# Performance work log

Measured on AMD Instinct MI355X. Metric: run time of the kernel, lower is better.

Reference implementation:

```python
import jax, jax.numpy as jnp
import numpy as np

B_BATCH, N_ATOMS, N_CGS = 128, 512, 16


def setup_inputs() -> dict:
    key = jax.random.key(0)
    k0, k1, k2, k3, k4, k5 = jax.random.split(key, 6)
    npair = N_CGS * N_CGS
    soft_assign = jax.random.uniform(k0, (B_BATCH, N_ATOMS, N_CGS), dtype=jnp.float32)
    a = jax.random.uniform(k1, (B_BATCH, N_ATOMS, N_CGS), dtype=jnp.float32)
    assign_norm = a / a.sum(axis=-1, keepdims=True)  # row-normalized soft assignment
    xyz = jax.random.normal(k2, (B_BATCH, N_ATOMS, 3), dtype=jnp.float32)
    cg_xyz = jax.random.normal(k3, (B_BATCH, N_CGS, 3), dtype=jnp.float32)
    W = 0.01 * jax.random.normal(k4, (N_ATOMS, npair + npair * npair), dtype=jnp.float32)
    assign_idx = jax.random.randint(k5, (N_ATOMS,), 0, N_CGS)
    return {"soft_assign": soft_assign, "xyz": xyz, "cg_xyz": cg_xyz,
            "assign_norm": assign_norm, "W": W, "assign_idx": assign_idx}


def reference(soft_assign, xyz, cg_xyz, assign_norm, W, assign_idx):
    b, n_cgs = cg_xyz.shape[0], cg_xyz.shape[1]
    npair = n_cgs * n_cgs
    # pairwise displacement basis: basis[b,i,j] = cg_xyz[b,j] - cg_xyz[b,i]
    basis = cg_xyz[:, None, :, :] - cg_xyz[:, :, None, :]      # [b, nc, nc, 3]
    Bmat = basis.reshape(b, npair, 3)                          # [b, npair, 3]
    # cross basis: entry (p,q) = cross(Bmat[q], Bmat[p]) (matches torch Bij x Bjk)
    cross_basis = jnp.cross(Bmat[:, None, :, :], Bmat[:, :, None, :])  # [b,npair,npair,3]
    Bfull = jnp.concatenate([Bmat, cross_basis.reshape(b, npair * npair, 3)], axis=1)
    # dx_recon[b,n,e] = sum_j Bfull[b,j,e] * W[n,j]
    dx_recon = jnp.einsum('bje,nj->bne', Bfull, W)             # [b, n_atoms, 3]
    # per-CG mean offset weighted by soft assignment
    cg_offset = jnp.einsum('bin,bij->bjn', dx_recon, assign_norm)  # [b, n_cgs, 3]
    xyz_recon = cg_xyz[:, assign_idx, :] - cg_offset[:, assign_idx, :] + dx_recon
    return (soft_assign, xyz, xyz_recon)
```

## Files before the change

### kernel.cpp

```cpp
#include <hip/hip_runtime.h>

constexpr int NC = 16;
constexpr int NP = 256;
constexpr int PITCH = 264;
constexpr int NATOMS = 512;
constexpr int NB = 128;
constexpr int WROW = NP + NP * NP;

__global__ __launch_bounds__(256) void k_stream(const float* __restrict__ W,
                                                const float* __restrict__ soft_assign,
                                                const float* __restrict__ xyz,
                                                float* __restrict__ wcd_part,
                                                float* __restrict__ out_sa,
                                                float* __restrict__ out_xyz) {
    __shared__ float Hl[NC][PITCH];
    const int bid = blockIdx.x;
    const int n = bid >> 1;
    const int half = bid & 1;
    const int t = threadIdx.x;

    ((float4*)out_sa)[bid * 256 + t] = ((const float4*)soft_assign)[bid * 256 + t];
    if (t < 48) {
        ((float4*)out_xyz)[bid * 48 + t] = ((const float4*)xyz)[bid * 48 + t];
    }

    const float* __restrict__ wp =
        W + (size_t)n * WROW + NP + (size_t)(half * 128) * NP + t;
    float h[NC];
#pragma unroll
    for (int d = 0; d < NC; ++d) h[d] = 0.f;
    float hn[8];
#pragma unroll
    for (int g = 0; g < 8; ++g) {
        float s = 0.f;
#pragma unroll
        for (int i = 0; i < 16; ++i) {
            const float v = wp[(size_t)(g * 16 + i) * NP];
            h[i] += v;
            s += v;
        }
        hn[g] = s;
    }
    if (half == 0) {
        h[0] -= hn[0]; h[1] -= hn[1]; h[2] -= hn[2]; h[3] -= hn[3];
        h[4] -= hn[4]; h[5] -= hn[5]; h[6] -= hn[6]; h[7] -= hn[7];
    } else {
        h[8]  -= hn[0]; h[9]  -= hn[1]; h[10] -= hn[2]; h[11] -= hn[3];
        h[12] -= hn[4]; h[13] -= hn[5]; h[14] -= hn[6]; h[15] -= hn[7];
    }

#pragma unroll
    for (int d = 0; d < NC; ++d) Hl[d][t] = h[d];
    __syncthreads();

    {
        const int d = t >> 4, c = t & 15;
        float rp = 0.f, rm = 0.f;
#pragma unroll
        for (int qi = 0; qi < NC; ++qi) rp += Hl[d][qi * NC + c];
#pragma unroll
        for (int qj = 0; qj < NC; ++qj) rm += Hl[d][c * NC + qj];
        wcd_part[((size_t)half * NATOMS + n) * NP + t] = rp - rm;
    }
}

__global__ __launch_bounds__(256) void k_sum(const float* __restrict__ wcd_part,
                                             const float* __restrict__ W,
                                             float* __restrict__ wcd,
                                             float* __restrict__ w1c) {
    const int n = blockIdx.x;
    const int t = threadIdx.x;
    const float a = wcd_part[(size_t)n * NP + t] +
                    wcd_part[((size_t)NATOMS + n) * NP + t];
    wcd[n * NP + t] = a;
    if (t < NC) {
        const float* __restrict__ W1 = W + (size_t)n * WROW;
        float a1 = 0.f;
#pragma unroll
        for (int pi = 0; pi < NC; ++pi) a1 += W1[pi * NC + t];
#pragma unroll
        for (int pj = 0; pj < NC; ++pj) a1 -= W1[t * NC + pj];
        w1c[n * NC + t] = a1;
    }
}

__global__ __launch_bounds__(512) void k_recon(const float* __restrict__ cg_xyz,
                                               const float* __restrict__ assign_norm,
                                               const int* __restrict__ assign_idx,
                                               const float* __restrict__ wcd,
                                               const float* __restrict__ w1c,
                                               float* __restrict__ out_recon) {
    __shared__ float xs[NC][4];
    __shared__ float cxs[NP][4];
    __shared__ float part[8][48];
    __shared__ float cgo[48];
    const int b = blockIdx.x;
    const int t = threadIdx.x;

    if (t < NC * 3) xs[t / 3][t % 3] = cg_xyz[(size_t)b * NC * 3 + t];
    __syncthreads();
    if (t < NP) {
        const int c = t & 15, d = t >> 4;
        const float ax = xs[c][0], ay = xs[c][1], az = xs[c][2];
        const float bx = xs[d][0], by = xs[d][1], bz = xs[d][2];
        cxs[t][0] = ay * bz - az * by;
        cxs[t][1] = az * bx - ax * bz;
        cxs[t][2] = ax * by - ay * bx;
        cxs[t][3] = 0.f;
    }
    __syncthreads();

    const int n = t;
    float dx0 = 0.f, dx1 = 0.f, dx2 = 0.f;
    const float4* __restrict__ wrow = (const float4*)(wcd + n * NP);
#pragma unroll 8
    for (int k4 = 0; k4 < 64; ++k4) {
        const float4 w = wrow[k4];
        const float4 c0 = *(const float4*)(&cxs[k4 * 4 + 0][0]);
        const float4 c1 = *(const float4*)(&cxs[k4 * 4 + 1][0]);
        const float4 c2 = *(const float4*)(&cxs[k4 * 4 + 2][0]);
        const float4 c3 = *(const float4*)(&cxs[k4 * 4 + 3][0]);
        dx0 += w.x * c0.x + w.y * c1.x + w.z * c2.x + w.w * c3.x;
        dx1 += w.x * c0.y + w.y * c1.y + w.z * c2.y + w.w * c3.y;
        dx2 += w.x * c0.z + w.y * c1.z + w.z * c2.z + w.w * c3.z;
    }
    const float* __restrict__ w1row = w1c + n * NC;
#pragma unroll
    for (int c = 0; c < NC; ++c) {
        const float wv = w1row[c];
        dx0 += wv * xs[c][0]; dx1 += wv * xs[c][1]; dx2 += wv * xs[c][2];
    }

    float an[NC];
    const float4* __restrict__ anr =
        (const float4*)(assign_norm + ((size_t)b * NATOMS + n) * NC);
#pragma unroll
    for (int i = 0; i < 4; ++i) {
        const float4 v = anr[i];
        an[4 * i + 0] = v.x; an[4 * i + 1] = v.y; an[4 * i + 2] = v.z; an[4 * i + 3] = v.w;
    }
    const int wv_ = t >> 6;
#pragma unroll
    for (int j = 0; j < NC; ++j) {
        float p0 = an[j] * dx0, p1 = an[j] * dx1, p2 = an[j] * dx2;
#pragma unroll
        for (int sh = 1; sh < 64; sh <<= 1) {
            p0 += __shfl_xor(p0, sh);
            p1 += __shfl_xor(p1, sh);
            p2 += __shfl_xor(p2, sh);
        }
        if ((t & 63) == 0) {
            part[wv_][j * 3 + 0] = p0;
            part[wv_][j * 3 + 1] = p1;
            part[wv_][j * 3 + 2] = p2;
        }
    }
    __syncthreads();
    if (t < 48) {
        float sm = 0.f;
#pragma unroll
        for (int w8 = 0; w8 < 8; ++w8) sm += part[w8][t];
        cgo[t] = sm;
    }
    __syncthreads();

    const int ci = assign_idx[n];
    const float r0 = xs[ci][0] - cgo[ci * 3 + 0] + dx0;
    const float r1 = xs[ci][1] - cgo[ci * 3 + 1] + dx1;
    const float r2 = xs[ci][2] - cgo[ci * 3 + 2] + dx2;
    const size_t ob = ((size_t)b * NATOMS + n) * 3;
    out_recon[ob + 0] = r0;
    out_recon[ob + 1] = r1;
    out_recon[ob + 2] = r2;
}

extern "C" void kernel_launch(void* const* d_in, const int* in_sizes, int n_in,
                              void* d_out, int out_size, void* d_ws, size_t ws_size,
                              hipStream_t stream) {
    (void)in_sizes; (void)n_in; (void)out_size; (void)ws_size;
    const float* soft_assign = (const float*)d_in[0];
    const float* xyz         = (const float*)d_in[1];
    const float* cg_xyz      = (const float*)d_in[2];
    const float* assign_norm = (const float*)d_in[3];
    const float* W           = (const float*)d_in[4];
    const int*   assign_idx  = (const int*)d_in[5];

    float* out       = (float*)d_out;
    float* out_sa    = out;
    float* out_xyz   = out + (size_t)NB * NATOMS * NC;
    float* out_recon = out_xyz + (size_t)NB * NATOMS * 3;

    float* wcd_part = (float*)d_ws;
    float* wcd      = wcd_part + (size_t)2 * NATOMS * NP;
    float* w1c      = wcd + (size_t)NATOMS * NP;

    k_stream<<<dim3(NATOMS * 2), dim3(256), 0, stream>>>(W, soft_assign, xyz,
                                                         wcd_part, out_sa, out_xyz);
    k_sum<<<dim3(NATOMS), dim3(256), 0, stream>>>(wcd_part, W, wcd, w1c);
    k_recon<<<dim3(NB), dim3(512), 0, stream>>>(cg_xyz, assign_norm, assign_idx,
                                                wcd, w1c, out_recon);
}
```

Before: 55.38 us.

## Split recon into parallel dx kernel over pair quarters and finish kernel

Moves the w1c computation into the streaming kernel and removes the separate k_sum pass, summing the two wcd halves inline. The dx matvec is spread over 512 blocks, each covering a quarter of the pair dimension, and writes partial dx values to workspace. A new finish kernel adds the partials and computes the per-CG offsets with an LDS-staged reduction instead of 16 full-wave shuffle reductions. This raises parallelism from 128 blocks, at the cost of extra workspace traffic and each wcd_part row being read by every batch block.

```diff
diff --git a/kernel.cpp b/kernel.cpp
--- a/kernel.cpp
+++ b/kernel.cpp
@@ -6,11 +6,14 @@
 constexpr int NATOMS = 512;
 constexpr int NB = 128;
 constexpr int WROW = NP + NP * NP;
+constexpr int ANP = 21;
+constexpr int DXP = 5;
 
 __global__ __launch_bounds__(256) void k_stream(const float* __restrict__ W,
                                                 const float* __restrict__ soft_assign,
                                                 const float* __restrict__ xyz,
                                                 float* __restrict__ wcd_part,
+                                                float* __restrict__ w1c,
                                                 float* __restrict__ out_sa,
                                                 float* __restrict__ out_xyz) {
     __shared__ float Hl[NC][PITCH];
@@ -24,6 +27,16 @@
         ((float4*)out_xyz)[bid * 48 + t] = ((const float4*)xyz)[bid * 48 + t];
     }
 
+    if (half == 0 && t < NC) {
+        const float* __restrict__ W1 = W + (size_t)n * WROW;
+        float a1 = 0.f;
+#pragma unroll
+        for (int pi = 0; pi < NC; ++pi) a1 += W1[pi * NC + t];
+#pragma unroll
+        for (int pj = 0; pj < NC; ++pj) a1 -= W1[t * NC + pj];
+        w1c[n * NC + t] = a1;
+    }
+
     const float* __restrict__ wp =
         W + (size_t)n * WROW + NP + (size_t)(half * 128) * NP + t;
     float h[NC];
@@ -64,43 +77,20 @@
     }
 }
 
-__global__ __launch_bounds__(256) void k_sum(const float* __restrict__ wcd_part,
-                                             const float* __restrict__ W,
-                                             float* __restrict__ wcd,
-                                             float* __restrict__ w1c) {
-    const int n = blockIdx.x;
+__global__ __launch_bounds__(256) void k_dx(const float* __restrict__ cg_xyz,
+                                            const float* __restrict__ wcd_part,
+                                            const float* __restrict__ w1c,
+                                            float* __restrict__ dxp) {
+    __shared__ float xs[NC][4];
+    __shared__ float cxs[64][4];
+    const int b = blockIdx.x >> 2;
+    const int q = blockIdx.x & 3;
     const int t = threadIdx.x;
-    const float a = wcd_part[(size_t)n * NP + t] +
-                    wcd_part[((size_t)NATOMS + n) * NP + t];
-    wcd[n * NP + t] = a;
-    if (t < NC) {
-        const float* __restrict__ W1 = W + (size_t)n * WROW;
-        float a1 = 0.f;
-#pragma unroll
-        for (int pi = 0; pi < NC; ++pi) a1 += W1[pi * NC + t];
-#pragma unroll
-        for (int pj = 0; pj < NC; ++pj) a1 -= W1[t * NC + pj];
-        w1c[n * NC + t] = a1;
-    }
-}
-
-__global__ __launch_bounds__(512) void k_recon(const float* __restrict__ cg_xyz,
-                                               const float* __restrict__ assign_norm,
-                                               const int* __restrict__ assign_idx,
-                                               const float* __restrict__ wcd,
-                                               const float* __restrict__ w1c,
-                                               float* __restrict__ out_recon) {
-    __shared__ float xs[NC][4];
-    __shared__ float cxs[NP][4];
-    __shared__ float part[8][48];
-    __shared__ float cgo[48];
-    const int b = blockIdx.x;
-    const int t = threadIdx.x;
-
-    if (t < NC * 3) xs[t / 3][t % 3] = cg_xyz[(size_t)b * NC * 3 + t];
-    __syncthreads();
-    if (t < NP) {
-        const int c = t & 15, d = t >> 4;
+
+    if (t < 48) xs[t / 3][t % 3] = cg_xyz[(size_t)b * NC * 3 + t];
+    __syncthreads();
+    if (t < 64) {
+        const int m = q * 64 + t, c = m & 15, d = m >> 4;
         const float ax = xs[c][0], ay = xs[c][1], az = xs[c][2];
         const float bx = xs[d][0], by = xs[d][1], bz = xs[d][2];
         cxs[t][0] = ay * bz - az * by;
@@ -110,65 +100,105 @@
     }
     __syncthreads();
 
-    const int n = t;
-    float dx0 = 0.f, dx1 = 0.f, dx2 = 0.f;
-    const float4* __restrict__ wrow = (const float4*)(wcd + n * NP);
-#pragma unroll 8
-    for (int k4 = 0; k4 < 64; ++k4) {
-        const float4 w = wrow[k4];
-        const float4 c0 = *(const float4*)(&cxs[k4 * 4 + 0][0]);
-        const float4 c1 = *(const float4*)(&cxs[k4 * 4 + 1][0]);
-        const float4 c2 = *(const float4*)(&cxs[k4 * 4 + 2][0]);
-        const float4 c3 = *(const float4*)(&cxs[k4 * 4 + 3][0]);
-        dx0 += w.x * c0.x + w.y * c1.x + w.z * c2.x + w.w * c3.x;
-        dx1 += w.x * c0.y + w.y * c1.y + w.z * c2.y + w.w * c3.y;
-        dx2 += w.x * c0.z + w.y * c1.z + w.z * c2.z + w.w * c3.z;
-    }
-    const float* __restrict__ w1row = w1c + n * NC;
-#pragma unroll
-    for (int c = 0; c < NC; ++c) {
-        const float wv = w1row[c];
-        dx0 += wv * xs[c][0]; dx1 += wv * xs[c][1]; dx2 += wv * xs[c][2];
-    }
-
-    float an[NC];
-    const float4* __restrict__ anr =
-        (const float4*)(assign_norm + ((size_t)b * NATOMS + n) * NC);
-#pragma unroll
-    for (int i = 0; i < 4; ++i) {
-        const float4 v = anr[i];
-        an[4 * i + 0] = v.x; an[4 * i + 1] = v.y; an[4 * i + 2] = v.z; an[4 * i + 3] = v.w;
-    }
-    const int wv_ = t >> 6;
-#pragma unroll
-    for (int j = 0; j < NC; ++j) {
-        float p0 = an[j] * dx0, p1 = an[j] * dx1, p2 = an[j] * dx2;
-#pragma unroll
-        for (int sh = 1; sh < 64; sh <<= 1) {
-            p0 += __shfl_xor(p0, sh);
-            p1 += __shfl_xor(p1, sh);
-            p2 += __shfl_xor(p2, sh);
-        }
-        if ((t & 63) == 0) {
-            part[wv_][j * 3 + 0] = p0;
-            part[wv_][j * 3 + 1] = p1;
-            part[wv_][j * 3 + 2] = p2;
-        }
-    }
-    __syncthreads();
-    if (t < 48) {
-        float sm = 0.f;
-#pragma unroll
-        for (int w8 = 0; w8 < 8; ++w8) sm += part[w8][t];
-        cgo[t] = sm;
-    }
-    __syncthreads();
-
-    const int ci = assign_idx[n];
-    const float r0 = xs[ci][0] - cgo[ci * 3 + 0] + dx0;
-    const float r1 = xs[ci][1] - cgo[ci * 3 + 1] + dx1;
-    const float r2 = xs[ci][2] - cgo[ci * 3 + 2] + dx2;
-    const size_t ob = ((size_t)b * NATOMS + n) * 3;
+#pragma unroll
+    for (int a = 0; a < 2; ++a) {
+        const int n = a * 256 + t;
+        const float4* __restrict__ w0 =
+            (const float4*)(wcd_part + (size_t)n * NP + q * 64);
+        const float4* __restrict__ w1 =
+            (const float4*)(wcd_part + ((size_t)NATOMS + n) * NP + q * 64);
+        float dx0 = 0.f, dx1 = 0.f, dx2 = 0.f;
+#pragma unroll
+        for (int k4 = 0; k4 < 16; ++k4) {
+            const float4 wa = w0[k4];
+            const float4 wb = w1[k4];
+            float4 w;
+            w.x = wa.x + wb.x; w.y = wa.y + wb.y;
+            w.z = wa.z + wb.z; w.w = wa.w + wb.w;
+            const float4 c0 = *(const float4*)(&cxs[k4 * 4 + 0][0]);
+            const float4 c1 = *(const float4*)(&cxs[k4 * 4 + 1][0]);
+            const float4 c2 = *(const float4*)(&cxs[k4 * 4 + 2][0]);
+            const float4 c3 = *(const float4*)(&cxs[k4 * 4 + 3][0]);
+            dx0 += w.x * c0.x + w.y * c1.x + w.z * c2.x + w.w * c3.x;
+            dx1 += w.x * c0.y + w.y * c1.y + w.z * c2.y + w.w * c3.y;
+            dx2 += w.x * c0.z + w.y * c1.z + w.z * c2.z + w.w * c3.z;
+        }
+        if (q == 0) {
+            const float* __restrict__ w1r = w1c + n * NC;
+#pragma unroll
+            for (int c = 0; c < NC; ++c) {
+                const float wv = w1r[c];
+                dx0 += wv * xs[c][0]; dx1 += wv * xs[c][1]; dx2 += wv * xs[c][2];
+            }
+        }
+        float* __restrict__ op = dxp + (((size_t)q * NB + b) * NATOMS + n) * 3;
+        op[0] = dx0; op[1] = dx1; op[2] = dx2;
+    }
+}
+
+__global__ __launch_bounds__(512) void k_finish(const float* __restrict__ cg_xyz,
+                                                const float* __restrict__ assign_norm,
+                                                const int* __restrict__ assign_idx,
+                                                const float* __restrict__ dxp,
+                                                float* __restrict__ out_recon) {
+    __shared__ float an_l[NATOMS][ANP];
+    __shared__ float dxl[NATOMS][DXP];
+    __shared__ float xs[NC][4];
+    __shared__ float cgo_l[NC][4];
+    const int b = blockIdx.x;
+    const int t = threadIdx.x;
+
+    {
+        const float4* __restrict__ anr =
+            (const float4*)(assign_norm + ((size_t)b * NATOMS + t) * NC);
+#pragma unroll
+        for (int i = 0; i < 4; ++i) {
+            const float4 v = anr[i];
+            an_l[t][4 * i + 0] = v.x; an_l[t][4 * i + 1] = v.y;
+            an_l[t][4 * i + 2] = v.z; an_l[t][4 * i + 3] = v.w;
+        }
+    }
+    if (t < 48) xs[t / 3][t % 3] = cg_xyz[(size_t)b * NC * 3 + t];
+
+    float dx0, dx1, dx2;
+    {
+        const size_t s0 = (((size_t)0 * NB + b) * NATOMS + t) * 3;
+        const size_t s1 = (((size_t)1 * NB + b) * NATOMS + t) * 3;
+        const size_t s2 = (((size_t)2 * NB + b) * NATOMS + t) * 3;
+        const size_t s3 = (((size_t)3 * NB + b) * NATOMS + t) * 3;
+        dx0 = (dxp[s0 + 0] + dxp[s1 + 0]) + (dxp[s2 + 0] + dxp[s3 + 0]);
+        dx1 = (dxp[s0 + 1] + dxp[s1 + 1]) + (dxp[s2 + 1] + dxp[s3 + 1]);
+        dx2 = (dxp[s0 + 2] + dxp[s1 + 2]) + (dxp[s2 + 2] + dxp[s3 + 2]);
+    }
+    dxl[t][0] = dx0; dxl[t][1] = dx1; dxl[t][2] = dx2;
+    __syncthreads();
+
+    {
+        const int j = t >> 5, g = t & 31;
+        float p0 = 0.f, p1 = 0.f, p2 = 0.f;
+#pragma unroll
+        for (int k = 0; k < 16; ++k) {
+            const int i = g + 32 * k;
+            const float a = an_l[i][j];
+            p0 += a * dxl[i][0];
+            p1 += a * dxl[i][1];
+            p2 += a * dxl[i][2];
+        }
+#pragma unroll
+        for (int s = 1; s < 32; s <<= 1) {
+            p0 += __shfl_xor(p0, s);
+            p1 += __shfl_xor(p1, s);
+            p2 += __shfl_xor(p2, s);
+        }
+        if (g == 0) { cgo_l[j][0] = p0; cgo_l[j][1] = p1; cgo_l[j][2] = p2; }
+    }
+    __syncthreads();
+
+    const int ci = assign_idx[t];
+    const float r0 = xs[ci][0] - cgo_l[ci][0] + dx0;
+    const float r1 = xs[ci][1] - cgo_l[ci][1] + dx1;
+    const float r2 = xs[ci][2] - cgo_l[ci][2] + dx2;
+    const size_t ob = ((size_t)b * NATOMS + t) * 3;
     out_recon[ob + 0] = r0;
     out_recon[ob + 1] = r1;
     out_recon[ob + 2] = r2;
@@ -191,12 +221,13 @@
     float* out_recon = out_xyz + (size_t)NB * NATOMS * 3;
 
     float* wcd_part = (float*)d_ws;
-    float* wcd      = wcd_part + (size_t)2 * NATOMS * NP;
-    float* w1c      = wcd + (size_t)NATOMS * NP;
+    float* w1c      = wcd_part + (size_t)2 * NATOMS * NP;
+    float* dxp      = w1c + (size_t)NATOMS * NC;
 
     k_stream<<<dim3(NATOMS * 2), dim3(256), 0, stream>>>(W, soft_assign, xyz,
-                                                         wcd_part, out_sa, out_xyz);
-    k_sum<<<dim3(NATOMS), dim3(256), 0, stream>>>(wcd_part, W, wcd, w1c);
-    k_recon<<<dim3(NB), dim3(512), 0, stream>>>(cg_xyz, assign_norm, assign_idx,
-                                                wcd, w1c, out_recon);
-}
+                                                         wcd_part, w1c,
+                                                         out_sa, out_xyz);
+    k_dx<<<dim3(NB * 4), dim3(256), 0, stream>>>(cg_xyz, wcd_part, w1c, dxp);
+    k_finish<<<dim3(NB), dim3(512), 0, stream>>>(cg_xyz, assign_norm, assign_idx,
+                                                 dxp, out_recon);
+}
```

Result: faster. 52.74 us (-4.8%).
